# Performance work log

Hardware: AMD Instinct MI355X
Metric: run time of the kernel (lower is better)

## Reference

```python
import jax, jax.numpy as jnp
import numpy as np

NUM_NODES = 100000
EMBED_DIM = 128
NUM_RELATIONS = 64
BATCH = 512


def setup_inputs() -> dict:
    key = jax.random.key(0)
    k1, k2, k3, k4, k5 = jax.random.split(key, 5)
    u = jax.random.randint(k1, (BATCH,), 0, NUM_NODES)
    v = jax.random.randint(k2, (BATCH,), 0, NUM_NODES)
    r = jax.random.randint(k3, (BATCH,), 0, NUM_RELATIONS)
    node_embeddings = jax.random.normal(k4, (NUM_NODES, EMBED_DIM), dtype=jnp.float32)
    relation_matrices = jax.random.normal(k5, (NUM_RELATIONS, EMBED_DIM, EMBED_DIM), dtype=jnp.float32)
    return {"u": u, "v": v, "r": r,
            "node_embeddings": node_embeddings,
            "relation_matrices": relation_matrices}


def reference(u, v, r, node_embeddings, relation_matrices):
    u_embed = node_embeddings[u]            # [B, D]
    v_embed = node_embeddings[v]            # [B, D]
    rel = relation_matrices[r]              # [B, D, D] per-sample gathered matrices
    # torch.matmul([B,D], [B,D,D]) broadcasts u_embed over the relation batch -> [B_rel, B_u, D]
    score = jnp.einsum('ud,bde->bue', u_embed, rel)   # [B, B, D]
    # matmul with v_embed.T [D, B] -> [B, B, B]
    score = jnp.einsum('bue,ve->buv', score, v_embed)  # [B, B, B]
    return jax.nn.sigmoid(score)
```

## Files before the change

### kernel.cpp

```cpp
#include <hip/hip_runtime.h>


#define BATCH 512
#define DIM   128
#define NRELS 64
#define NTHR  256

typedef float floatx4 __attribute__((ext_vector_type(4)));

__device__ __forceinline__ void lds_barrier() {
    asm volatile("s_waitcnt lgkmcnt(0)" ::: "memory");
    __builtin_amdgcn_s_barrier();
    __builtin_amdgcn_sched_barrier(0);
}

__global__ __launch_bounds__(NTHR, 2)
void rad_fused_kernel(const int* __restrict__ u_idx,
                      const int* __restrict__ v_idx,
                      const int* __restrict__ r_idx,
                      const float* __restrict__ nodes,
                      const float* __restrict__ rels,
                      float* __restrict__ out)
{
    const int bid = (int)blockIdx.x;
    const int rel = ((bid & 7) << 3) | (bid >> 6);
    const int ut0 = ((bid >> 3) & 7) * 64;

    __shared__ int s_match[BATCH];
    __shared__ int s_mc;
    __shared__ __align__(16) float s_TsT[DIM * 64];
    __shared__ __align__(16) float s_buf[DIM * 64 + 16 * DIM];

    const int t  = (int)threadIdx.x;
    const int tu = t >> 4;
    const int tx = t & 15;

    if (t == 0) s_mc = 0;
    __syncthreads();
    for (int i = t; i < BATCH; i += NTHR) {
        if (r_idx[i] == rel) {
            int p = atomicAdd(&s_mc, 1);
            s_match[p] = i;
        }
    }

    float* UEsT = s_buf;
    float* Rs   = s_buf + DIM * 64;

    for (int i = t; i < 64 * (DIM / 4); i += NTHR) {
        const int row = i & 63;
        const int dc  = i >> 6;
        const float4 val = *reinterpret_cast<const float4*>(
            nodes + (size_t)u_idx[ut0 + row] * DIM + dc * 4);
        UEsT[(dc * 4 + 0) * 64 + row] = val.x;
        UEsT[(dc * 4 + 1) * 64 + row] = val.y;
        UEsT[(dc * 4 + 2) * 64 + row] = val.z;
        UEsT[(dc * 4 + 3) * 64 + row] = val.w;
    }
    __syncthreads();
    const int mc = s_mc;
    if (mc == 0) return;

    float accA[4][8];
    #pragma unroll
    for (int i = 0; i < 4; ++i)
        #pragma unroll
        for (int j = 0; j < 8; ++j) accA[i][j] = 0.f;

    const float* Rbase = rels + (size_t)rel * DIM * DIM;
    for (int dch = 0; dch < DIM / 16; ++dch) {
        for (int i = t; i < 16 * (DIM / 4); i += NTHR) {
            const int rr = i >> 5;
            const int cc = i & 31;
            *reinterpret_cast<float4*>(Rs + rr * DIM + cc * 4) =
                *reinterpret_cast<const float4*>(
                    Rbase + (size_t)(dch * 16 + rr) * DIM + cc * 4);
        }
        lds_barrier();
        #pragma unroll
        for (int dd = 0; dd < 16; ++dd) {
            const int d = dch * 16 + dd;
            const float4 a  = *reinterpret_cast<const float4*>(UEsT + d * 64 + tu * 4);
            const float4 b0 = *reinterpret_cast<const float4*>(Rs + dd * DIM + tx * 4);
            const float4 b1 = *reinterpret_cast<const float4*>(Rs + dd * DIM + 64 + tx * 4);
            const float av[4] = {a.x, a.y, a.z, a.w};
            const float bv[8] = {b0.x, b0.y, b0.z, b0.w, b1.x, b1.y, b1.z, b1.w};
            #pragma unroll
            for (int i = 0; i < 4; ++i)
                #pragma unroll
                for (int j = 0; j < 8; ++j)
                    accA[i][j] = fmaf(av[i], bv[j], accA[i][j]);
        }
        lds_barrier();
    }

    #pragma unroll
    for (int j = 0; j < 8; ++j) {
        const int e = (j < 4) ? (tx * 4 + j) : (64 + tx * 4 + (j - 4));
        #pragma unroll
        for (int i = 0; i < 4; ++i)
            s_TsT[e * 64 + tu * 4 + i] = accA[i][j];
    }

    float* VEsT = s_buf;
    for (int vt = 0; vt < BATCH / 64; ++vt) {
        lds_barrier();
        for (int i = t; i < 64 * (DIM / 4); i += NTHR) {
            const int row = i & 63;
            const int ec  = i >> 6;
            const float4 val = *reinterpret_cast<const float4*>(
                nodes + (size_t)v_idx[vt * 64 + row] * DIM + ec * 4);
            VEsT[(ec * 4 + 0) * 64 + row] = val.x;
            VEsT[(ec * 4 + 1) * 64 + row] = val.y;
            VEsT[(ec * 4 + 2) * 64 + row] = val.z;
            VEsT[(ec * 4 + 3) * 64 + row] = val.w;
        }
        lds_barrier();

        float acc[4][4];
        #pragma unroll
        for (int i = 0; i < 4; ++i)
            #pragma unroll
            for (int j = 0; j < 4; ++j) acc[i][j] = 0.f;

        #pragma unroll 8
        for (int e = 0; e < DIM; ++e) {
            const float4 a = *reinterpret_cast<const float4*>(s_TsT + e * 64 + tu * 4);
            const float4 b = *reinterpret_cast<const float4*>(VEsT  + e * 64 + tx * 4);
            const float av[4] = {a.x, a.y, a.z, a.w};
            const float bv[4] = {b.x, b.y, b.z, b.w};
            #pragma unroll
            for (int i = 0; i < 4; ++i)
                #pragma unroll
                for (int j = 0; j < 4; ++j)
                    acc[i][j] = fmaf(av[i], bv[j], acc[i][j]);
        }

        floatx4 sg[4];
        #pragma unroll
        for (int i = 0; i < 4; ++i) {
            sg[i].x = 1.f / (1.f + __expf(-acc[i][0]));
            sg[i].y = 1.f / (1.f + __expf(-acc[i][1]));
            sg[i].z = 1.f / (1.f + __expf(-acc[i][2]));
            sg[i].w = 1.f / (1.f + __expf(-acc[i][3]));
        }

        for (int m = 0; m < mc; ++m) {
            const int bb = s_match[m];
            float* obase = out + (size_t)bb * BATCH * BATCH + vt * 64 + tx * 4;
            #pragma unroll
            for (int i = 0; i < 4; ++i) {
                *reinterpret_cast<floatx4*>(
                    obase + (size_t)(ut0 + tu * 4 + i) * BATCH) = sg[i];
            }
        }
    }
}

extern "C" void kernel_launch(void* const* d_in, const int* in_sizes, int n_in,
                              void* d_out, int out_size, void* d_ws, size_t ws_size,
                              hipStream_t stream) {
    const int*   u_idx = (const int*)d_in[0];
    const int*   v_idx = (const int*)d_in[1];
    const int*   r_idx = (const int*)d_in[2];
    const float* nodes = (const float*)d_in[3];
    const float* rels  = (const float*)d_in[4];
    float* out = (float*)d_out;

    dim3 grid(NRELS * 8);
    dim3 block(NTHR);
    rad_fused_kernel<<<grid, block, 0, stream>>>(u_idx, v_idx, r_idx, nodes, rels, out);
}
```

Baseline: 149.5 us.

## Shrink u-tile to 16 rows, stage sigmoid slab in LDS, write contiguous rows

Each block now handles 16 u rows instead of 64, so the grid grows to 2048 blocks. Each block computes the whole 16x512 sigmoid slab into LDS, then writes it once per matching relation as fully contiguous 2 KB output rows. The aim is better occupancy and load spread, plus streaming output stores, since the kernel is bound by writing the 512 MB output. The cost is that R is reloaded 4x as often, v embeddings are re-gathered by 4x as many blocks, and each thread's inner products have lower register reuse.

```diff
diff --git a/kernel.cpp b/kernel.cpp
--- a/kernel.cpp
+++ b/kernel.cpp
@@ -5,7 +5,10 @@
 #define DIM   128
 #define NRELS 64
 #define NTHR  256
+#define UROWS 16
+#define SROW  (BATCH + 4)
 
+typedef float floatx2 __attribute__((ext_vector_type(2)));
 typedef float floatx4 __attribute__((ext_vector_type(4)));
 
 __device__ __forceinline__ void lds_barrier() {
@@ -15,24 +18,27 @@
 }
 
 __global__ __launch_bounds__(NTHR, 2)
-void rad_fused_kernel(const int* __restrict__ u_idx,
-                      const int* __restrict__ v_idx,
-                      const int* __restrict__ r_idx,
-                      const float* __restrict__ nodes,
-                      const float* __restrict__ rels,
-                      float* __restrict__ out)
+void rad_slab_kernel(const int* __restrict__ u_idx,
+                     const int* __restrict__ v_idx,
+                     const int* __restrict__ r_idx,
+                     const float* __restrict__ nodes,
+                     const float* __restrict__ rels,
+                     float* __restrict__ out)
 {
     const int bid = (int)blockIdx.x;
-    const int rel = ((bid & 7) << 3) | (bid >> 6);
-    const int ut0 = ((bid >> 3) & 7) * 64;
+    const int x   = bid & 7;
+    const int k   = bid >> 3;
+    const int rel = k >> 2;
+    const int ut0 = (((k & 3) << 3) | x) << 4;
 
     __shared__ int s_match[BATCH];
     __shared__ int s_mc;
-    __shared__ __align__(16) float s_TsT[DIM * 64];
-    __shared__ __align__(16) float s_buf[DIM * 64 + 16 * DIM];
+    __shared__ __align__(16) float TsT[DIM * UROWS];
+    __shared__ __align__(16) float S[UROWS * SROW];
+    __shared__ __align__(16) float buf[DIM * 64];
 
     const int t  = (int)threadIdx.x;
-    const int tu = t >> 4;
+    const int r  = t >> 4;
     const int tx = t & 15;
 
     if (t == 0) s_mc = 0;
@@ -44,28 +50,26 @@
         }
     }
 
-    float* UEsT = s_buf;
-    float* Rs   = s_buf + DIM * 64;
+    float* UEsT = buf;
+    float* Rs   = buf + DIM * UROWS;
 
-    for (int i = t; i < 64 * (DIM / 4); i += NTHR) {
-        const int row = i & 63;
-        const int dc  = i >> 6;
+    for (int i = t; i < UROWS * (DIM / 4); i += NTHR) {
+        const int row = i & 15;
+        const int dc  = i >> 4;
         const float4 val = *reinterpret_cast<const float4*>(
             nodes + (size_t)u_idx[ut0 + row] * DIM + dc * 4);
-        UEsT[(dc * 4 + 0) * 64 + row] = val.x;
-        UEsT[(dc * 4 + 1) * 64 + row] = val.y;
-        UEsT[(dc * 4 + 2) * 64 + row] = val.z;
-        UEsT[(dc * 4 + 3) * 64 + row] = val.w;
+        UEsT[(dc * 4 + 0) * UROWS + row] = val.x;
+        UEsT[(dc * 4 + 1) * UROWS + row] = val.y;
+        UEsT[(dc * 4 + 2) * UROWS + row] = val.z;
+        UEsT[(dc * 4 + 3) * UROWS + row] = val.w;
     }
     __syncthreads();
     const int mc = s_mc;
     if (mc == 0) return;
 
-    float accA[4][8];
+    float accA[8];
     #pragma unroll
-    for (int i = 0; i < 4; ++i)
-        #pragma unroll
-        for (int j = 0; j < 8; ++j) accA[i][j] = 0.f;
+    for (int j = 0; j < 8; ++j) accA[j] = 0.f;
 
     const float* Rbase = rels + (size_t)rel * DIM * DIM;
     for (int dch = 0; dch < DIM / 16; ++dch) {
@@ -80,29 +84,27 @@
         #pragma unroll
         for (int dd = 0; dd < 16; ++dd) {
             const int d = dch * 16 + dd;
-            const float4 a  = *reinterpret_cast<const float4*>(UEsT + d * 64 + tu * 4);
+            const float a  = UEsT[d * UROWS + r];
             const float4 b0 = *reinterpret_cast<const float4*>(Rs + dd * DIM + tx * 4);
             const float4 b1 = *reinterpret_cast<const float4*>(Rs + dd * DIM + 64 + tx * 4);
-            const float av[4] = {a.x, a.y, a.z, a.w};
-            const float bv[8] = {b0.x, b0.y, b0.z, b0.w, b1.x, b1.y, b1.z, b1.w};
-            #pragma unroll
-            for (int i = 0; i < 4; ++i)
-                #pragma unroll
-                for (int j = 0; j < 8; ++j)
-                    accA[i][j] = fmaf(av[i], bv[j], accA[i][j]);
+            accA[0] = fmaf(a, b0.x, accA[0]);
+            accA[1] = fmaf(a, b0.y, accA[1]);
+            accA[2] = fmaf(a, b0.z, accA[2]);
+            accA[3] = fmaf(a, b0.w, accA[3]);
+            accA[4] = fmaf(a, b1.x, accA[4]);
+            accA[5] = fmaf(a, b1.y, accA[5]);
+            accA[6] = fmaf(a, b1.z, accA[6]);
+            accA[7] = fmaf(a, b1.w, accA[7]);
         }
         lds_barrier();
     }
-
     #pragma unroll
     for (int j = 0; j < 8; ++j) {
-        const int e = (j < 4) ? (tx * 4 + j) : (64 + tx * 4 + (j - 4));
-        #pragma unroll
-        for (int i = 0; i < 4; ++i)
-            s_TsT[e * 64 + tu * 4 + i] = accA[i][j];
+        const int e = tx * 4 + (j & 3) + 64 * (j >> 2);
+        TsT[e * UROWS + r] = accA[j];
     }
 
-    float* VEsT = s_buf;
+    float* VEsT = buf;
     for (int vt = 0; vt < BATCH / 64; ++vt) {
         lds_barrier();
         for (int i = t; i < 64 * (DIM / 4); i += NTHR) {
@@ -117,42 +119,43 @@
         }
         lds_barrier();
 
-        float acc[4][4];
-        #pragma unroll
-        for (int i = 0; i < 4; ++i)
-            #pragma unroll
-            for (int j = 0; j < 4; ++j) acc[i][j] = 0.f;
-
+        float a0 = 0.f, a1 = 0.f, a2 = 0.f, a3 = 0.f;
         #pragma unroll 8
         for (int e = 0; e < DIM; ++e) {
-            const float4 a = *reinterpret_cast<const float4*>(s_TsT + e * 64 + tu * 4);
-            const float4 b = *reinterpret_cast<const float4*>(VEsT  + e * 64 + tx * 4);
-            const float av[4] = {a.x, a.y, a.z, a.w};
-            const float bv[4] = {b.x, b.y, b.z, b.w};
+            const float  a = TsT[e * UROWS + r];
+            const float4 b = *reinterpret_cast<const float4*>(VEsT + e * 64 + tx * 4);
+            a0 = fmaf(a, b.x, a0);
+            a1 = fmaf(a, b.y, a1);
+            a2 = fmaf(a, b.z, a2);
+            a3 = fmaf(a, b.w, a3);
+        }
+        float4 sg;
+        sg.x = 1.f / (1.f + __expf(-a0));
+        sg.y = 1.f / (1.f + __expf(-a1));
+        sg.z = 1.f / (1.f + __expf(-a2));
+        sg.w = 1.f / (1.f + __expf(-a3));
+        *reinterpret_cast<float4*>(S + r * SROW + vt * 64 + tx * 4) = sg;
+    }
+
+    const int w = t >> 6;
+    const int l = t & 63;
+    floatx2 rv[4][4];
+    #pragma unroll
+    for (int rr = 0; rr < 4; ++rr)
+        #pragma unroll
+        for (int c = 0; c < 4; ++c)
+            rv[rr][c] = *reinterpret_cast<const floatx2*>(
+                S + (w * 4 + rr) * SROW + c * 128 + 2 * l);
+
+    for (int m = 0; m < mc; ++m) {
+        const int bb = s_match[m];
+        float* ob = out + ((size_t)bb << 18) + ((size_t)ut0 << 9);
+        #pragma unroll
+        for (int rr = 0; rr < 4; ++rr) {
+            float* orow = ob + ((size_t)(w * 4 + rr) << 9) + 2 * l;
             #pragma unroll
-            for (int i = 0; i < 4; ++i)
-                #pragma unroll
-                for (int j = 0; j < 4; ++j)
-                    acc[i][j] = fmaf(av[i], bv[j], acc[i][j]);
-        }
-
-        floatx4 sg[4];
-        #pragma unroll
-        for (int i = 0; i < 4; ++i) {
-            sg[i].x = 1.f / (1.f + __expf(-acc[i][0]));
-            sg[i].y = 1.f / (1.f + __expf(-acc[i][1]));
-            sg[i].z = 1.f / (1.f + __expf(-acc[i][2]));
-            sg[i].w = 1.f / (1.f + __expf(-acc[i][3]));
-        }
-
-        for (int m = 0; m < mc; ++m) {
-            const int bb = s_match[m];
-            float* obase = out + (size_t)bb * BATCH * BATCH + vt * 64 + tx * 4;
-            #pragma unroll
-            for (int i = 0; i < 4; ++i) {
-                *reinterpret_cast<floatx4*>(
-                    obase + (size_t)(ut0 + tu * 4 + i) * BATCH) = sg[i];
-            }
+            for (int c = 0; c < 4; ++c)
+                *reinterpret_cast<floatx2*>(orow + c * 128) = rv[rr][c];
         }
     }
 }
@@ -167,7 +170,7 @@
     const float* rels  = (const float*)d_in[4];
     float* out = (float*)d_out;
 
-    dim3 grid(NRELS * 8);
+    dim3 grid(NRELS * 32);
     dim3 block(NTHR);
-    rad_fused_kernel<<<grid, block, 0, stream>>>(u_idx, v_idx, r_idx, nodes, rels, out);
+    rad_slab_kernel<<<grid, block, 0, stream>>>(u_idx, v_idx, r_idx, nodes, rels, out);
 }
```

Measured after the change: 282.5 us. 89.0% more time.
